# Optimization experiments

Measured on AMD Instinct MI355X. Metric: run time of the kernel, lower is better.

## Reference

```python
import jax, jax.numpy as jnp
import numpy as np

N, C, H, W = 32, 512, 32, 32
D = C // 2  # theta/phi embed channels


def setup_inputs() -> dict:
    key = jax.random.key(0)
    ks = jax.random.split(key, 7)
    s = 0.05
    return {
        "x": jax.random.normal(ks[0], (N, C, H, W), jnp.float32),
        "W_theta": jax.random.normal(ks[1], (D, C), jnp.float32) * s,
        "b_theta": jax.random.normal(ks[2], (D,), jnp.float32) * s,
        "W_phi": jax.random.normal(ks[3], (D, C), jnp.float32) * s,
        "b_phi": jax.random.normal(ks[4], (D,), jnp.float32) * s,
        "W_fuse": jax.random.normal(ks[5], (C, C), jnp.float32) * s,
        "b_fuse": jax.random.normal(ks[6], (C,), jnp.float32) * s,
    }


def _conv1x1(x, Wt, bt):
    # 1x1 conv == per-pixel linear: [n,c,h,w] x [o,c] -> [n,o,h,w]
    return jnp.einsum('nchw,oc->nohw', x, Wt) + bt[None, :, None, None]


def reference(x, W_theta, b_theta, W_phi, b_phi, W_fuse, b_fuse):
    n, c, h, w = x.shape
    theta = _conv1x1(x, W_theta, b_theta)          # [n, d, h, w]
    phi = _conv1x1(x, W_phi, b_phi)                # [n, d, h, w]
    d = theta.shape[1]
    hw = h * w
    t = theta.reshape(n, d, hw)                    # queries [n, d, hw]
    p = phi.reshape(n, d, hw)                      # keys    [n, d, hw]
    g = x.reshape(n, c, hw)                        # values  [n, c, hw]
    scale = 1.0 / np.sqrt(float(d))
    f = jnp.einsum('ndq,ndk->nqk', t, p) * scale   # [n, hw, hw]
    f = jax.nn.softmax(f, axis=-1)
    attn = jnp.einsum('nqk,nck->ncq', f, g).reshape(n, c, h, w)
    return x + _conv1x1(attn, W_fuse, b_fuse)
```

## Files before the change

### kernel.cpp

```cpp
#include <hip/hip_runtime.h>


#define NB  32
#define CC  512
#define HWD 1024

typedef __attribute__((ext_vector_type(8))) short short8;
typedef __attribute__((ext_vector_type(4))) float f32x4;

__device__ __forceinline__ unsigned short f2bu(float f) {
    unsigned int u = __float_as_uint(f);
    u = (u + 0x7FFFu + ((u >> 16) & 1u)) >> 16;
    return (unsigned short)u;
}

__global__ __launch_bounds__(256) void k_packw(const float* __restrict__ Wt,
                                               const float* __restrict__ Wp,
                                               const float* __restrict__ Wf,
                                               unsigned short* __restrict__ Wcat,
                                               unsigned short* __restrict__ Wfuse) {
    int idx = blockIdx.x * 256 + threadIdx.x;
    int o = idx >> 9;
    float cv = (o < 256) ? Wt[idx] : Wp[idx - 131072];
    Wcat[idx]  = f2bu(cv);
    Wfuse[idx] = f2bu(Wf[idx]);
}

__global__ __launch_bounds__(512) void k_mm(const float* __restrict__ x,
                                            const unsigned short* __restrict__ Wcat,
                                            const unsigned short* __restrict__ Wfuse,
                                            const float* __restrict__ bt,
                                            const float* __restrict__ bp,
                                            unsigned short* __restrict__ tp,
                                            unsigned short* __restrict__ Z) {
    __shared__ __align__(16) float Tr[32 * 132];
    __shared__ __align__(16) unsigned short As[128 * 40];
    __shared__ __align__(16) unsigned short Bs[256 * 40];
    const int m0 = blockIdx.x << 7;
    const int yb = blockIdx.y;
    const bool isZ = (yb >= 2);
    const int n0 = (yb & 1) << 8;
    const unsigned short* W = isZ ? Wfuse : Wcat;
    const int n  = m0 >> 10, qbase = m0 & 1023;
    const int t = threadIdx.x, lane = t & 63, wave = t >> 6;
    const int wr = wave >> 2, wc = wave & 3;
    const int lrow = lane & 15, hi = lane >> 4, lhk = hi << 3;
    const f32x4 fz = {0.f, 0.f, 0.f, 0.f};
    f32x4 acc[4][4];
#pragma unroll
    for (int i = 0; i < 4; ++i)
#pragma unroll
        for (int j = 0; j < 4; ++j) acc[i][j] = fz;

    const int tr_r = t >> 4, tr_q = (t & 15) << 3;
    const int p2_pix = t & 127, p2_c = (t >> 7) << 3;

    for (int kt = 0; kt < 16; ++kt) {
        const int k0 = kt << 5;
        {
            const float* src = x + ((size_t)(n * CC + k0 + tr_r)) * HWD + qbase + tr_q;
            float4 v0 = *(const float4*)(src);
            float4 v1 = *(const float4*)(src + 4);
            *(float4*)(Tr + tr_r * 132 + tr_q) = v0;
            *(float4*)(Tr + tr_r * 132 + tr_q + 4) = v1;
#pragma unroll
            for (int i = 0; i < 2; ++i) {
                int chunk = t + (i << 9);
                int r = chunk >> 2, ko = (chunk & 3) << 3;
                *(uint4*)(Bs + r * 40 + ko) =
                    *(const uint4*)(W + ((size_t)(n0 + r)) * CC + k0 + ko);
            }
        }
        __syncthreads();
        {
            short8 o8;
#pragma unroll
            for (int j = 0; j < 8; ++j)
                o8[j] = (short)f2bu(Tr[(p2_c + j) * 132 + p2_pix]);
            *(short8*)(As + p2_pix * 40 + p2_c) = o8;
        }
        __syncthreads();
        short8 af[4], bfm[4];
#pragma unroll
        for (int mi = 0; mi < 4; ++mi)
            af[mi] = *(const short8*)(As + (wr * 64 + mi * 16 + lrow) * 40 + lhk);
#pragma unroll
        for (int ni = 0; ni < 4; ++ni)
            bfm[ni] = *(const short8*)(Bs + (wc * 64 + ni * 16 + lrow) * 40 + lhk);
#pragma unroll
        for (int mi = 0; mi < 4; ++mi)
#pragma unroll
            for (int ni = 0; ni < 4; ++ni)
                acc[mi][ni] = __builtin_amdgcn_mfma_f32_16x16x32_bf16(
                    af[mi], bfm[ni], acc[mi][ni], 0, 0, 0);
        __syncthreads();
    }
    if (!isZ) {
#pragma unroll
        for (int ni = 0; ni < 4; ++ni) {
            const int col = n0 + wc * 64 + ni * 16 + lrow;
            const float bias = (col < 256) ? bt[col] : bp[col - 256];
#pragma unroll
            for (int mi = 0; mi < 4; ++mi)
#pragma unroll
                for (int j = 0; j < 4; ++j) {
                    const int row = m0 + wr * 64 + mi * 16 + hi * 4 + j;
                    tp[(size_t)row * CC + col] = f2bu(acc[mi][ni][j] + bias);
                }
        }
    } else {
        const int kbase = qbase + wr * 64;
        unsigned short* Zn = Z + (size_t)n * CC * HWD;
#pragma unroll
        for (int ni = 0; ni < 4; ++ni) {
            const int o = n0 + wc * 64 + ni * 16 + lrow;
#pragma unroll
            for (int mi = 0; mi < 4; ++mi) {
                ushort4 v;
                v.x = f2bu(acc[mi][ni][0]);
                v.y = f2bu(acc[mi][ni][1]);
                v.z = f2bu(acc[mi][ni][2]);
                v.w = f2bu(acc[mi][ni][3]);
                *(ushort4*)(Zn + (size_t)o * HWD + kbase + mi * 16 + (hi << 2)) = v;
            }
        }
    }
}

__global__ __launch_bounds__(512, 2) void k_attn8(const unsigned short* __restrict__ tp,
                                                  const unsigned short* __restrict__ Z,
                                                  const float* __restrict__ bfu,
                                                  const float* __restrict__ x,
                                                  float* __restrict__ out) {
    constexpr int QST = 264;
    constexpr int PST = 264;
    constexpr int QSZ = 128 * QST;
    __shared__ __align__(16) unsigned short SL[QSZ + 128 * PST];
    __shared__ float rowsum[128];
    unsigned short* Qs = SL;
    unsigned short* P  = SL + QSZ;

    const int b = blockIdx.x;
    const int n = b & 31;
    const int q0 = (b >> 5) << 7;
    const int t = threadIdx.x, lane = t & 63, wave = t >> 6;
    const int lrow = lane & 15, hi = lane >> 4, lhk = hi << 3;
    const f32x4 fz = {0.f, 0.f, 0.f, 0.f};

    const unsigned short* tpn = tp + (size_t)n * HWD * CC;
    const unsigned short* Zn  = Z + (size_t)n * CC * HWD;

    if (t < 128) rowsum[t] = 0.f;
#pragma unroll
    for (int pass = 0; pass < 8; ++pass) {
        int chunk = (pass << 9) + t;
        int row = chunk >> 5, co = (chunk & 31) << 3;
        *(short8*)(Qs + row * QST + co) =
            *(const short8*)(tpn + (size_t)(q0 + row) * CC + co);
    }
    __syncthreads();

    f32x4 accG[8][4];
#pragma unroll
    for (int qj = 0; qj < 8; ++qj)
#pragma unroll
        for (int mi = 0; mi < 4; ++mi) accG[qj][mi] = fz;

    const int kw = wave << 4;
    const int ob = wave << 6;

    for (int it = 0; it < 4; ++it) {
        const int kv0 = it << 8;
        const size_t krow0 = (size_t)(kv0 + kw + lrow) * CC + 256;
        const size_t krow1 = (size_t)(kv0 + 128 + kw + lrow) * CC + 256;
        f32x4 accA[2][8];
#pragma unroll
        for (int k2 = 0; k2 < 2; ++k2)
#pragma unroll
            for (int qj = 0; qj < 8; ++qj) accA[k2][qj] = fz;
#pragma unroll
        for (int kt = 0; kt < 8; ++kt) {
            const int d0 = (kt << 5) + lhk;
            short8 kf0 = *(const short8*)(tpn + krow0 + d0);
            short8 kf1 = *(const short8*)(tpn + krow1 + d0);
#pragma unroll
            for (int qj = 0; qj < 8; ++qj) {
                short8 qfr = *(const short8*)(Qs + (qj * 16 + lrow) * QST + d0);
                accA[0][qj] = __builtin_amdgcn_mfma_f32_16x16x32_bf16(qfr, kf0, accA[0][qj], 0, 0, 0);
                accA[1][qj] = __builtin_amdgcn_mfma_f32_16x16x32_bf16(qfr, kf1, accA[1][qj], 0, 0, 0);
            }
        }
        float psum[8][4];
#pragma unroll
        for (int qj = 0; qj < 8; ++qj)
#pragma unroll
            for (int j = 0; j < 4; ++j) psum[qj][j] = 0.f;
#pragma unroll
        for (int k2 = 0; k2 < 2; ++k2) {
            const int pcol = (k2 << 7) + kw + lrow;
#pragma unroll
            for (int qj = 0; qj < 8; ++qj)
#pragma unroll
                for (int j = 0; j < 4; ++j) {
                    float p = __expf(accA[k2][qj][j] * 0.0625f);
                    psum[qj][j] += p;
                    P[(qj * 16 + hi * 4 + j) * PST + pcol] = f2bu(p);
                }
        }
#pragma unroll
        for (int qj = 0; qj < 8; ++qj)
#pragma unroll
            for (int j = 0; j < 4; ++j) {
                float s = psum[qj][j];
                s += __shfl_xor(s, 1, 16);
                s += __shfl_xor(s, 2, 16);
                s += __shfl_xor(s, 4, 16);
                s += __shfl_xor(s, 8, 16);
                if (lrow == 0) atomicAdd(&rowsum[qj * 16 + hi * 4 + j], s);
            }
        __syncthreads();
        __builtin_amdgcn_s_setprio(1);
#pragma unroll
        for (int ks = 0; ks < 8; ++ks) {
            const int kb = (ks << 5) + lhk;
            short8 zf[4];
#pragma unroll
            for (int mi = 0; mi < 4; ++mi)
                zf[mi] = *(const short8*)(Zn + (size_t)(ob + mi * 16 + lrow) * HWD + kv0 + kb);
#pragma unroll
            for (int qj = 0; qj < 8; ++qj) {
                short8 pa = *(const short8*)(P + (qj * 16 + lrow) * PST + kb);
#pragma unroll
                for (int mi = 0; mi < 4; ++mi)
                    accG[qj][mi] = __builtin_amdgcn_mfma_f32_16x16x32_bf16(
                        pa, zf[mi], accG[qj][mi], 0, 0, 0);
            }
        }
        __builtin_amdgcn_s_setprio(0);
        __syncthreads();
    }

    if (t < 128) rowsum[t] = 1.f / rowsum[t];
    __syncthreads();
    float bias[4];
#pragma unroll
    for (int mi = 0; mi < 4; ++mi) bias[mi] = bfu[ob + mi * 16 + lrow];
#pragma unroll
    for (int qj = 0; qj < 8; ++qj) {
        const float4 inv4 = *(const float4*)&rowsum[qj * 16 + (hi << 2)];
#pragma unroll
        for (int mi = 0; mi < 4; ++mi) {
            const int o = ob + mi * 16 + lrow;
            const size_t idx = ((size_t)(n * CC + o)) * HWD + q0 + qj * 16 + (hi << 2);
            const float4 xr = *(const float4*)(x + idx);
            float4 r;
            r.x = accG[qj][mi][0] * inv4.x + bias[mi] + xr.x;
            r.y = accG[qj][mi][1] * inv4.y + bias[mi] + xr.y;
            r.z = accG[qj][mi][2] * inv4.z + bias[mi] + xr.z;
            r.w = accG[qj][mi][3] * inv4.w + bias[mi] + xr.w;
            *(float4*)(out + idx) = r;
        }
    }
}

extern "C" void kernel_launch(void* const* d_in, const int* in_sizes, int n_in,
                              void* d_out, int out_size, void* d_ws, size_t ws_size,
                              hipStream_t stream) {
    const float* x  = (const float*)d_in[0];
    const float* Wt = (const float*)d_in[1];
    const float* bt = (const float*)d_in[2];
    const float* Wp = (const float*)d_in[3];
    const float* bp = (const float*)d_in[4];
    const float* Wf = (const float*)d_in[5];
    const float* bfu = (const float*)d_in[6];
    float* out = (float*)d_out;

    char* ws = (char*)d_ws;
    unsigned short* tp    = (unsigned short*)(ws);
    unsigned short* Z     = (unsigned short*)(ws + 33554432);
    unsigned short* Wcat  = (unsigned short*)(ws + 67108864);
    unsigned short* Wfuse = (unsigned short*)(ws + 67633152);

    k_packw<<<dim3(1024), 256, 0, stream>>>(Wt, Wp, Wf, Wcat, Wfuse);
    k_mm   <<<dim3(256, 4), 512, 0, stream>>>(x, Wcat, Wfuse, bt, bp, tp, Z);
    k_attn8<<<dim3(256), 512, 0, stream>>>(tp, Z, bfu, x, out);
}
```

Baseline: 170.4 us.

## Store fused values and softmax probabilities in FP8 for PV MFMA

Converts the precomputed fused-value tensor Z and the per-tile softmax probabilities from bf16 to FP8 e4m3, and runs the P·Z product with fp8 MFMA instructions. Exponentials are shifted by a constant and clamped to the e4m3 range, and the P tile in LDS gets an XOR swizzle with a new stride. The aim is to halve Z's global traffic and LDS footprint and use higher-throughput fp8 matrix ops. In exchange, precision drops noticeably. The fixed exp offset without a running max risks overflow or underflow if logits fall outside the expected range.

```diff
diff --git a/kernel.cpp b/kernel.cpp
--- a/kernel.cpp
+++ b/kernel.cpp
@@ -13,6 +13,21 @@
     u = (u + 0x7FFFu + ((u >> 16) & 1u)) >> 16;
     return (unsigned short)u;
 }
+
+__device__ __forceinline__ unsigned char f2e4m3(float f) {
+    unsigned int u = __float_as_uint(f);
+    unsigned int s = (u >> 24) & 0x80u;
+    u &= 0x7FFFFFFFu;
+    if (u > 0x43E00000u) u = 0x43E00000u;
+    u += 0x0007FFFFu + ((u >> 20) & 1u);
+    int e = (int)(u >> 23) - 120;
+    unsigned char b = (e <= 0) ? (unsigned char)0
+                               : (unsigned char)((e << 3) | ((u >> 20) & 7u));
+    return (unsigned char)(b | s);
+}
+
+#define PSTB 272
+#define PSWZ(row, col) ((row) * PSTB + (((col) ^ (((row) & 7) << 4))))
 
 __global__ __launch_bounds__(256) void k_packw(const float* __restrict__ Wt,
                                                const float* __restrict__ Wp,
@@ -32,7 +47,7 @@
                                             const float* __restrict__ bt,
                                             const float* __restrict__ bp,
                                             unsigned short* __restrict__ tp,
-                                            unsigned short* __restrict__ Z) {
+                                            unsigned char* __restrict__ Z8) {
     __shared__ __align__(16) float Tr[32 * 132];
     __shared__ __align__(16) unsigned short As[128 * 40];
     __shared__ __align__(16) unsigned short Bs[256 * 40];
@@ -110,35 +125,34 @@
         }
     } else {
         const int kbase = qbase + wr * 64;
-        unsigned short* Zn = Z + (size_t)n * CC * HWD;
+        unsigned char* Zn = Z8 + (size_t)n * CC * HWD;
 #pragma unroll
         for (int ni = 0; ni < 4; ++ni) {
             const int o = n0 + wc * 64 + ni * 16 + lrow;
 #pragma unroll
             for (int mi = 0; mi < 4; ++mi) {
-                ushort4 v;
-                v.x = f2bu(acc[mi][ni][0]);
-                v.y = f2bu(acc[mi][ni][1]);
-                v.z = f2bu(acc[mi][ni][2]);
-                v.w = f2bu(acc[mi][ni][3]);
-                *(ushort4*)(Zn + (size_t)o * HWD + kbase + mi * 16 + (hi << 2)) = v;
-            }
-        }
-    }
-}
-
-__global__ __launch_bounds__(512, 2) void k_attn8(const unsigned short* __restrict__ tp,
-                                                  const unsigned short* __restrict__ Z,
-                                                  const float* __restrict__ bfu,
-                                                  const float* __restrict__ x,
-                                                  float* __restrict__ out) {
+                uchar4 v;
+                v.x = f2e4m3(acc[mi][ni][0]);
+                v.y = f2e4m3(acc[mi][ni][1]);
+                v.z = f2e4m3(acc[mi][ni][2]);
+                v.w = f2e4m3(acc[mi][ni][3]);
+                *(uchar4*)(Zn + (size_t)o * HWD + kbase + mi * 16 + (hi << 2)) = v;
+            }
+        }
+    }
+}
+
+__global__ __launch_bounds__(512, 2) void k_attn11(const unsigned short* __restrict__ tp,
+                                                   const unsigned char* __restrict__ Z8,
+                                                   const float* __restrict__ bfu,
+                                                   const float* __restrict__ x,
+                                                   float* __restrict__ out) {
     constexpr int QST = 264;
-    constexpr int PST = 264;
-    constexpr int QSZ = 128 * QST;
-    __shared__ __align__(16) unsigned short SL[QSZ + 128 * PST];
+    constexpr int QSZB = 128 * QST * 2;
+    __shared__ __align__(16) unsigned char SLB[QSZB + 128 * PSTB];
     __shared__ float rowsum[128];
-    unsigned short* Qs = SL;
-    unsigned short* P  = SL + QSZ;
+    unsigned short* Qs = (unsigned short*)SLB;
+    unsigned char*  P8 = SLB + QSZB;
 
     const int b = blockIdx.x;
     const int n = b & 31;
@@ -148,7 +162,7 @@
     const f32x4 fz = {0.f, 0.f, 0.f, 0.f};
 
     const unsigned short* tpn = tp + (size_t)n * HWD * CC;
-    const unsigned short* Zn  = Z + (size_t)n * CC * HWD;
+    const unsigned char*  Zn  = Z8 + (size_t)n * CC * HWD;
 
     if (t < 128) rowsum[t] = 0.f;
 #pragma unroll
@@ -202,9 +216,10 @@
             for (int qj = 0; qj < 8; ++qj)
 #pragma unroll
                 for (int j = 0; j < 4; ++j) {
-                    float p = __expf(accA[k2][qj][j] * 0.0625f);
+                    float p = __expf(accA[k2][qj][j] * 0.0625f - 2.0f);
+                    p = fminf(p, 448.f);
                     psum[qj][j] += p;
-                    P[(qj * 16 + hi * 4 + j) * PST + pcol] = f2bu(p);
+                    P8[PSWZ(qj * 16 + hi * 4 + j, pcol)] = f2e4m3(p);
                 }
         }
 #pragma unroll
@@ -221,19 +236,27 @@
         __syncthreads();
         __builtin_amdgcn_s_setprio(1);
 #pragma unroll
-        for (int ks = 0; ks < 8; ++ks) {
-            const int kb = (ks << 5) + lhk;
-            short8 zf[4];
-#pragma unroll
-            for (int mi = 0; mi < 4; ++mi)
-                zf[mi] = *(const short8*)(Zn + (size_t)(ob + mi * 16 + lrow) * HWD + kv0 + kb);
+        for (int win = 0; win < 4; ++win) {
+            const int kb = kv0 + (win << 6) + (hi << 4);
+            long zlo[4], zhi[4];
+#pragma unroll
+            for (int mi = 0; mi < 4; ++mi) {
+                uint4 zv = *(const uint4*)(Zn + (size_t)(ob + mi * 16 + lrow) * HWD + kb);
+                zlo[mi] = (long)(((unsigned long)zv.y << 32) | zv.x);
+                zhi[mi] = (long)(((unsigned long)zv.w << 32) | zv.z);
+            }
 #pragma unroll
             for (int qj = 0; qj < 8; ++qj) {
-                short8 pa = *(const short8*)(P + (qj * 16 + lrow) * PST + kb);
-#pragma unroll
-                for (int mi = 0; mi < 4; ++mi)
-                    accG[qj][mi] = __builtin_amdgcn_mfma_f32_16x16x32_bf16(
-                        pa, zf[mi], accG[qj][mi], 0, 0, 0);
+                uint4 pv = *(const uint4*)(P8 + PSWZ(qj * 16 + lrow, (win << 6) + (hi << 4)));
+                long plo = (long)(((unsigned long)pv.y << 32) | pv.x);
+                long phi = (long)(((unsigned long)pv.w << 32) | pv.z);
+#pragma unroll
+                for (int mi = 0; mi < 4; ++mi) {
+                    accG[qj][mi] = __builtin_amdgcn_mfma_f32_16x16x32_fp8_fp8(
+                        plo, zlo[mi], accG[qj][mi], 0, 0, 0);
+                    accG[qj][mi] = __builtin_amdgcn_mfma_f32_16x16x32_fp8_fp8(
+                        phi, zhi[mi], accG[qj][mi], 0, 0, 0);
+                }
             }
         }
         __builtin_amdgcn_s_setprio(0);
@@ -277,11 +300,11 @@
 
     char* ws = (char*)d_ws;
     unsigned short* tp    = (unsigned short*)(ws);
-    unsigned short* Z     = (unsigned short*)(ws + 33554432);
+    unsigned char*  Z8    = (unsigned char*)(ws + 33554432);
     unsigned short* Wcat  = (unsigned short*)(ws + 67108864);
     unsigned short* Wfuse = (unsigned short*)(ws + 67633152);
 
-    k_packw<<<dim3(1024), 256, 0, stream>>>(Wt, Wp, Wf, Wcat, Wfuse);
-    k_mm   <<<dim3(256, 4), 512, 0, stream>>>(x, Wcat, Wfuse, bt, bp, tp, Z);
-    k_attn8<<<dim3(256), 512, 0, stream>>>(tp, Z, bfu, x, out);
-}
+    k_packw <<<dim3(1024), 256, 0, stream>>>(Wt, Wp, Wf, Wcat, Wfuse);
+    k_mm    <<<dim3(256, 4), 512, 0, stream>>>(x, Wcat, Wfuse, bt, bp, tp, Z8);
+    k_attn11<<<dim3(256), 512, 0, stream>>>(tp, Z8, bfu, x, out);
+}
```

New measurement: 216.3 us. 1.27x slower.

## Double-buffer Z slices into LDS via async global_load_lds; read Q from global

Applied to the files above, without the earlier changes.

The attention kernel now stages each 32-column slice of the fused-value matrix Z into a double-buffered LDS region with global_load_lds. The next slice is prefetched while the current one feeds the MFMAs, synchronised with explicit vmcnt waits. To make room in LDS, the Q tile is no longer cached in shared memory and is read straight from global memory inside the score loop. This trades more global traffic for Q (mostly L2-cached) against hiding Z load latency. The manual waitcnt handling is fragile, and no barrier orders the cross-wave LDS writes before reads, although each wave reads only the rows it staged itself.

```diff
diff --git a/kernel.cpp b/kernel.cpp
--- a/kernel.cpp
+++ b/kernel.cpp
@@ -127,18 +127,18 @@
     }
 }
 
-__global__ __launch_bounds__(512, 2) void k_attn8(const unsigned short* __restrict__ tp,
-                                                  const unsigned short* __restrict__ Z,
-                                                  const float* __restrict__ bfu,
-                                                  const float* __restrict__ x,
-                                                  float* __restrict__ out) {
-    constexpr int QST = 264;
+__global__ __launch_bounds__(512, 2) void k_attn12(const unsigned short* __restrict__ tp,
+                                                   const unsigned short* __restrict__ Z,
+                                                   const float* __restrict__ bfu,
+                                                   const float* __restrict__ x,
+                                                   float* __restrict__ out) {
     constexpr int PST = 264;
-    constexpr int QSZ = 128 * QST;
-    __shared__ __align__(16) unsigned short SL[QSZ + 128 * PST];
+    constexpr int PSZB = 128 * PST * 2;
+    constexpr int ZBUF = 512 * 32;
+    __shared__ __align__(16) unsigned char SLB[PSZB + 2 * ZBUF * 2];
     __shared__ float rowsum[128];
-    unsigned short* Qs = SL;
-    unsigned short* P  = SL + QSZ;
+    unsigned short* P  = (unsigned short*)SLB;
+    unsigned short* ZB = (unsigned short*)(SLB + PSZB);
 
     const int b = blockIdx.x;
     const int n = b & 31;
@@ -150,14 +150,23 @@
     const unsigned short* tpn = tp + (size_t)n * HWD * CC;
     const unsigned short* Zn  = Z + (size_t)n * CC * HWD;
 
+    const int srl = lane >> 2, scl = lane & 3;
+    auto stage_slice = [&](int g) {
+        const int rbase = wave << 6;
+        unsigned short* lbase = ZB + (size_t)(g & 1) * ZBUF;
+#pragma unroll
+        for (int i = 0; i < 4; ++i) {
+            const unsigned short* gsrc =
+                Zn + (size_t)(rbase + (i << 4) + srl) * HWD + g * 32 + scl * 8;
+            unsigned short* ldst = lbase + (size_t)(rbase + (i << 4)) * 32;
+            __builtin_amdgcn_global_load_lds(
+                (__attribute__((address_space(1))) void*)(void*)const_cast<unsigned short*>(gsrc),
+                (__attribute__((address_space(3))) void*)ldst, 16, 0, 0);
+        }
+    };
+
     if (t < 128) rowsum[t] = 0.f;
-#pragma unroll
-    for (int pass = 0; pass < 8; ++pass) {
-        int chunk = (pass << 9) + t;
-        int row = chunk >> 5, co = (chunk & 31) << 3;
-        *(short8*)(Qs + row * QST + co) =
-            *(const short8*)(tpn + (size_t)(q0 + row) * CC + co);
-    }
+    stage_slice(0);
     __syncthreads();
 
     f32x4 accG[8][4];
@@ -185,7 +194,7 @@
             short8 kf1 = *(const short8*)(tpn + krow1 + d0);
 #pragma unroll
             for (int qj = 0; qj < 8; ++qj) {
-                short8 qfr = *(const short8*)(Qs + (qj * 16 + lrow) * QST + d0);
+                short8 qfr = *(const short8*)(tpn + (size_t)(q0 + qj * 16 + lrow) * CC + d0);
                 accA[0][qj] = __builtin_amdgcn_mfma_f32_16x16x32_bf16(qfr, kf0, accA[0][qj], 0, 0, 0);
                 accA[1][qj] = __builtin_amdgcn_mfma_f32_16x16x32_bf16(qfr, kf1, accA[1][qj], 0, 0, 0);
             }
@@ -222,11 +231,20 @@
         __builtin_amdgcn_s_setprio(1);
 #pragma unroll
         for (int ks = 0; ks < 8; ++ks) {
+            const int g = (it << 3) + ks;
+            if (g + 1 < 32) stage_slice(g + 1);
+            if (g + 1 < 32) {
+                asm volatile("s_waitcnt vmcnt(4)" ::: "memory");
+            } else {
+                asm volatile("s_waitcnt vmcnt(0)" ::: "memory");
+            }
+            __builtin_amdgcn_sched_barrier(0);
+            const unsigned short* zb = ZB + (size_t)(g & 1) * ZBUF;
+            short8 zf[4];
+#pragma unroll
+            for (int mi = 0; mi < 4; ++mi)
+                zf[mi] = *(const short8*)(zb + (size_t)(ob + mi * 16 + lrow) * 32 + lhk);
             const int kb = (ks << 5) + lhk;
-            short8 zf[4];
-#pragma unroll
-            for (int mi = 0; mi < 4; ++mi)
-                zf[mi] = *(const short8*)(Zn + (size_t)(ob + mi * 16 + lrow) * HWD + kv0 + kb);
 #pragma unroll
             for (int qj = 0; qj < 8; ++qj) {
                 short8 pa = *(const short8*)(P + (qj * 16 + lrow) * PST + kb);
@@ -281,7 +299,7 @@
     unsigned short* Wcat  = (unsigned short*)(ws + 67108864);
     unsigned short* Wfuse = (unsigned short*)(ws + 67633152);
 
-    k_packw<<<dim3(1024), 256, 0, stream>>>(Wt, Wp, Wf, Wcat, Wfuse);
-    k_mm   <<<dim3(256, 4), 512, 0, stream>>>(x, Wcat, Wfuse, bt, bp, tp, Z);
-    k_attn8<<<dim3(256), 512, 0, stream>>>(tp, Z, bfu, x, out);
-}
+    k_packw <<<dim3(1024), 256, 0, stream>>>(Wt, Wp, Wf, Wcat, Wfuse);
+    k_mm    <<<dim3(256, 4), 512, 0, stream>>>(x, Wcat, Wfuse, bt, bp, tp, Z);
+    k_attn12<<<dim3(256), 512, 0, stream>>>(tp, Z, bfu, x, out);
+}
```

New measurement: 284.9 us. +67.1%, slower.

## Split attention block work across 16 waves instead of 8

Applied to the files above, without the earlier changes.

The attention kernel now launches 1024 threads per block (16 waves). Each wave computes scores for 16 keys instead of 32 and accumulates 32 output channels instead of 64. This halves per-wave accumulator registers and raises the number of waves available to hide latency per CU. In exchange, each wave does less MFMA work between barriers, Q fragments are re-read from LDS by twice as many waves, and atomics on the row sums increase. The launch bound of (1024, 4) may also force register spilling.

```diff
diff --git a/kernel.cpp b/kernel.cpp
--- a/kernel.cpp
+++ b/kernel.cpp
@@ -127,11 +127,11 @@
     }
 }
 
-__global__ __launch_bounds__(512, 2) void k_attn8(const unsigned short* __restrict__ tp,
-                                                  const unsigned short* __restrict__ Z,
-                                                  const float* __restrict__ bfu,
-                                                  const float* __restrict__ x,
-                                                  float* __restrict__ out) {
+__global__ __launch_bounds__(1024, 4) void k_attn13(const unsigned short* __restrict__ tp,
+                                                    const unsigned short* __restrict__ Z,
+                                                    const float* __restrict__ bfu,
+                                                    const float* __restrict__ x,
+                                                    float* __restrict__ out) {
     constexpr int QST = 264;
     constexpr int PST = 264;
     constexpr int QSZ = 128 * QST;
@@ -152,86 +152,73 @@
 
     if (t < 128) rowsum[t] = 0.f;
 #pragma unroll
-    for (int pass = 0; pass < 8; ++pass) {
-        int chunk = (pass << 9) + t;
+    for (int pass = 0; pass < 4; ++pass) {
+        int chunk = (pass << 10) + t;
         int row = chunk >> 5, co = (chunk & 31) << 3;
         *(short8*)(Qs + row * QST + co) =
             *(const short8*)(tpn + (size_t)(q0 + row) * CC + co);
     }
     __syncthreads();
 
-    f32x4 accG[8][4];
+    f32x4 accG[8][2];
 #pragma unroll
     for (int qj = 0; qj < 8; ++qj)
 #pragma unroll
-        for (int mi = 0; mi < 4; ++mi) accG[qj][mi] = fz;
+        for (int mi = 0; mi < 2; ++mi) accG[qj][mi] = fz;
 
     const int kw = wave << 4;
-    const int ob = wave << 6;
+    const int ob = wave << 5;
 
     for (int it = 0; it < 4; ++it) {
         const int kv0 = it << 8;
-        const size_t krow0 = (size_t)(kv0 + kw + lrow) * CC + 256;
-        const size_t krow1 = (size_t)(kv0 + 128 + kw + lrow) * CC + 256;
-        f32x4 accA[2][8];
-#pragma unroll
-        for (int k2 = 0; k2 < 2; ++k2)
-#pragma unroll
-            for (int qj = 0; qj < 8; ++qj) accA[k2][qj] = fz;
+        const size_t krow = (size_t)(kv0 + kw + lrow) * CC + 256;
+        f32x4 accA[8];
+#pragma unroll
+        for (int qj = 0; qj < 8; ++qj) accA[qj] = fz;
 #pragma unroll
         for (int kt = 0; kt < 8; ++kt) {
             const int d0 = (kt << 5) + lhk;
-            short8 kf0 = *(const short8*)(tpn + krow0 + d0);
-            short8 kf1 = *(const short8*)(tpn + krow1 + d0);
+            short8 kf = *(const short8*)(tpn + krow + d0);
 #pragma unroll
             for (int qj = 0; qj < 8; ++qj) {
                 short8 qfr = *(const short8*)(Qs + (qj * 16 + lrow) * QST + d0);
-                accA[0][qj] = __builtin_amdgcn_mfma_f32_16x16x32_bf16(qfr, kf0, accA[0][qj], 0, 0, 0);
-                accA[1][qj] = __builtin_amdgcn_mfma_f32_16x16x32_bf16(qfr, kf1, accA[1][qj], 0, 0, 0);
-            }
-        }
-        float psum[8][4];
-#pragma unroll
-        for (int qj = 0; qj < 8; ++qj)
-#pragma unroll
-            for (int j = 0; j < 4; ++j) psum[qj][j] = 0.f;
-#pragma unroll
-        for (int k2 = 0; k2 < 2; ++k2) {
-            const int pcol = (k2 << 7) + kw + lrow;
-#pragma unroll
-            for (int qj = 0; qj < 8; ++qj)
-#pragma unroll
-                for (int j = 0; j < 4; ++j) {
-                    float p = __expf(accA[k2][qj][j] * 0.0625f);
-                    psum[qj][j] += p;
-                    P[(qj * 16 + hi * 4 + j) * PST + pcol] = f2bu(p);
-                }
-        }
-#pragma unroll
-        for (int qj = 0; qj < 8; ++qj)
+                accA[qj] = __builtin_amdgcn_mfma_f32_16x16x32_bf16(qfr, kf, accA[qj], 0, 0, 0);
+            }
+        }
+        const int pcol = kw + lrow;
+#pragma unroll
+        for (int qj = 0; qj < 8; ++qj) {
+            float ps[4];
 #pragma unroll
             for (int j = 0; j < 4; ++j) {
-                float s = psum[qj][j];
+                float p = __expf(accA[qj][j] * 0.0625f);
+                ps[j] = p;
+                P[(qj * 16 + hi * 4 + j) * PST + pcol] = f2bu(p);
+            }
+#pragma unroll
+            for (int j = 0; j < 4; ++j) {
+                float s = ps[j];
                 s += __shfl_xor(s, 1, 16);
                 s += __shfl_xor(s, 2, 16);
                 s += __shfl_xor(s, 4, 16);
                 s += __shfl_xor(s, 8, 16);
                 if (lrow == 0) atomicAdd(&rowsum[qj * 16 + hi * 4 + j], s);
             }
+        }
         __syncthreads();
         __builtin_amdgcn_s_setprio(1);
 #pragma unroll
         for (int ks = 0; ks < 8; ++ks) {
             const int kb = (ks << 5) + lhk;
-            short8 zf[4];
-#pragma unroll
-            for (int mi = 0; mi < 4; ++mi)
+            short8 zf[2];
+#pragma unroll
+            for (int mi = 0; mi < 2; ++mi)
                 zf[mi] = *(const short8*)(Zn + (size_t)(ob + mi * 16 + lrow) * HWD + kv0 + kb);
 #pragma unroll
             for (int qj = 0; qj < 8; ++qj) {
                 short8 pa = *(const short8*)(P + (qj * 16 + lrow) * PST + kb);
 #pragma unroll
-                for (int mi = 0; mi < 4; ++mi)
+                for (int mi = 0; mi < 2; ++mi)
                     accG[qj][mi] = __builtin_amdgcn_mfma_f32_16x16x32_bf16(
                         pa, zf[mi], accG[qj][mi], 0, 0, 0);
             }
@@ -242,14 +229,14 @@
 
     if (t < 128) rowsum[t] = 1.f / rowsum[t];
     __syncthreads();
-    float bias[4];
-#pragma unroll
-    for (int mi = 0; mi < 4; ++mi) bias[mi] = bfu[ob + mi * 16 + lrow];
+    float bias[2];
+#pragma unroll
+    for (int mi = 0; mi < 2; ++mi) bias[mi] = bfu[ob + mi * 16 + lrow];
 #pragma unroll
     for (int qj = 0; qj < 8; ++qj) {
         const float4 inv4 = *(const float4*)&rowsum[qj * 16 + (hi << 2)];
 #pragma unroll
-        for (int mi = 0; mi < 4; ++mi) {
+        for (int mi = 0; mi < 2; ++mi) {
             const int o = ob + mi * 16 + lrow;
             const size_t idx = ((size_t)(n * CC + o)) * HWD + q0 + qj * 16 + (hi << 2);
             const float4 xr = *(const float4*)(x + idx);
@@ -281,7 +268,7 @@
     unsigned short* Wcat  = (unsigned short*)(ws + 67108864);
     unsigned short* Wfuse = (unsigned short*)(ws + 67633152);
 
-    k_packw<<<dim3(1024), 256, 0, stream>>>(Wt, Wp, Wf, Wcat, Wfuse);
-    k_mm   <<<dim3(256, 4), 512, 0, stream>>>(x, Wcat, Wfuse, bt, bp, tp, Z);
-    k_attn8<<<dim3(256), 512, 0, stream>>>(tp, Z, bfu, x, out);
-}
+    k_packw <<<dim3(1024), 256, 0, stream>>>(Wt, Wp, Wf, Wcat, Wfuse);
+    k_mm    <<<dim3(256, 4), 512, 0, stream>>>(x, Wcat, Wfuse, bt, bp, tp, Z);
+    k_attn13<<<dim3(256), 1024, 0, stream>>>(tp, Z, bfu, x, out);
+}
```

New measurement: 198.1 us. 16.2% more time.
